# Performance work log

Hardware: AMD Instinct MI355X
Metric: run time of the kernel (lower is better)

## Reference

```python
import jax, jax.numpy as jnp
import numpy as np

T, B, I, H, O = 512, 64, 256, 512, 256

def setup_inputs() -> dict:
    key = jax.random.key(0)
    ks = jax.random.split(key, 7)
    s_ih = 1.0 / np.sqrt(H)
    return {
        "x": jax.random.normal(ks[0], (T, B, I), dtype=jnp.float32),
        "W_ih": jax.random.uniform(ks[1], (H, I), jnp.float32, -s_ih, s_ih),
        "W_hh": jax.random.uniform(ks[2], (H, H), jnp.float32, -s_ih, s_ih),
        "b_ih": jax.random.uniform(ks[3], (H,), jnp.float32, -s_ih, s_ih),
        "b_hh": jax.random.uniform(ks[4], (H,), jnp.float32, -s_ih, s_ih),
        "W_out": jax.random.uniform(ks[5], (O, H), jnp.float32, -s_ih, s_ih),
        "b_out": jax.random.uniform(ks[6], (O,), jnp.float32, -s_ih, s_ih),
    }

def reference(x, W_ih, W_hh, b_ih, b_hh, W_out, b_out):
    # Precompute input projection for all timesteps: [T, B, H]
    xp = jnp.einsum('tbi,hi->tbh', x, W_ih) + b_ih + b_hh

    def step(h, xp_t):
        h_new = jnp.tanh(xp_t + h @ W_hh.T)
        return h_new, h_new

    h0 = jnp.zeros((x.shape[1], W_hh.shape[0]), dtype=x.dtype)
    h_last, rnn_out = jax.lax.scan(step, h0, xp)  # rnn_out: [T, B, H]
    y = jnp.einsum('tbh,oh->tbo', rnn_out, W_out) + b_out
    return y, h_last[None]  # h: [1, B, H] matching torch nn.RNN
```

## Files before the change

kernel.cpp:

```cpp
#include <hip/hip_runtime.h>

#define T_DIM 512
#define B_DIM 64
#define I_DIM 256
#define H_DIM 512
#define O_DIM 256

typedef __attribute__((ext_vector_type(8))) short short8;
typedef __attribute__((ext_vector_type(4))) float f32x4;

__device__ __forceinline__ unsigned short f2bf(float f){
  unsigned int u = __builtin_bit_cast(unsigned int, f);
  u += 0x7fffu + ((u >> 16) & 1u);
  return (unsigned short)(u >> 16);
}
__device__ __forceinline__ float bf2f(unsigned short b){
  unsigned int u = ((unsigned int)b) << 16;
  return __builtin_bit_cast(float, u);
}

#if defined(__has_builtin)
#if __has_builtin(__builtin_amdgcn_sdot4)
#define HAVE_SDOT4 1
#endif
#if __has_builtin(__builtin_amdgcn_update_dpp)
#define HAVE_DPP 1
#endif
#endif

__device__ __forceinline__ int sdot4(int a, int b, int c){
#ifdef HAVE_SDOT4
  return __builtin_amdgcn_sdot4(a, b, c, false);
#else
  #pragma unroll
  for (int i = 0; i < 4; ++i){
    c += (int)(signed char)(a >> (8*i) & 0xff) * (int)(signed char)(b >> (8*i) & 0xff);
  }
  return c;
#endif
}

__device__ __forceinline__ int grp8_sum(int v){
#ifdef HAVE_DPP
  v += __builtin_amdgcn_update_dpp(0, v, 0xB1, 0xf, 0xf, true);
  v += __builtin_amdgcn_update_dpp(0, v, 0x4E, 0xf, 0xf, true);
  v += __builtin_amdgcn_update_dpp(0, v, 0x141, 0xf, 0xf, true);
  return v;
#else
  v += __shfl_xor(v, 1);
  v += __shfl_xor(v, 2);
  v += __shfl_xor(v, 4);
  return v;
#endif
}

__global__ void quant_whh(const float* __restrict__ W, int* __restrict__ Wq){
  int p = blockIdx.x * blockDim.x + threadIdx.x;
  const float s  = 0.04419417382415922f;
  const float qs = 127.0f / s;
  int out = 0;
  #pragma unroll
  for (int i = 0; i < 4; ++i){
    float w = W[(size_t)p*4 + i];
    int q = __float2int_rn(w * qs);
    q = q < -127 ? -127 : (q > 127 ? 127 : q);
    out |= (q & 0xff) << (8*i);
  }
  Wq[p] = out;
}

#define PIN16(i) asm volatile("" \
  : "+v"(w[i][ 0]), "+v"(w[i][ 1]), "+v"(w[i][ 2]), "+v"(w[i][ 3]), \
    "+v"(w[i][ 4]), "+v"(w[i][ 5]), "+v"(w[i][ 6]), "+v"(w[i][ 7]), \
    "+v"(w[i][ 8]), "+v"(w[i][ 9]), "+v"(w[i][10]), "+v"(w[i][11]), \
    "+v"(w[i][12]), "+v"(w[i][13]), "+v"(w[i][14]), "+v"(w[i][15]))

__global__
__attribute__((amdgpu_flat_work_group_size(512, 512), amdgpu_waves_per_eu(2, 2)))
void rnn_recur(
    const int* __restrict__ Wq,
    const unsigned short* __restrict__ xp,
    unsigned short* __restrict__ rnn,
    float* __restrict__ hlast)
{
  __shared__ union {
    int  hq[2][128];
    char occupancy_cap[84 * 1024];
  } sm;
  const int b   = blockIdx.x;
  const int tid = threadIdx.x;
  const int g   = tid >> 3;
  const int c   = tid & 7;

  int w[8][16];
  #pragma unroll
  for (int i = 0; i < 8; ++i){
    const uint4* wp = (const uint4*)(Wq + (size_t)(8*g + i)*128 + c*16);
    #pragma unroll
    for (int k = 0; k < 4; ++k){
      uint4 v = wp[k];
      w[i][4*k+0] = (int)v.x; w[i][4*k+1] = (int)v.y;
      w[i][4*k+2] = (int)v.z; w[i][4*k+3] = (int)v.w;
    }
  }
  if (tid < 256) ((int*)sm.hq)[tid] = 0;

  const int D = tid >> 2;
  const int wq_idx = ((D >> 4) + 8*((D >> 2) & 3))*4 + (D & 3);

  const float kscale = 0.04419417382415922f / (127.0f * 127.0f);
  const int BH = B_DIM * H_DIM;

  float xp_next = bf2f(xp[(size_t)b*H_DIM + tid]);
  __syncthreads();

  for (int t = 0; t < T_DIM; ++t){
    PIN16(0); PIN16(1); PIN16(2); PIN16(3);
    PIN16(4); PIN16(5); PIN16(6); PIN16(7);

    float xp_cur = xp_next;
    {
      int tn = (t + 1 < T_DIM) ? (t + 1) : t;
      xp_next = bf2f(xp[(size_t)tn*BH + (size_t)b*H_DIM + tid]);
    }
    const uint4* hb = (const uint4*)sm.hq[t & 1];
    uint4 hv0 = hb[c];
    uint4 hv1 = hb[c + 8];
    uint4 hv2 = hb[c + 16];
    uint4 hv3 = hb[c + 24];

    int acc[8];
    #pragma unroll
    for (int i = 0; i < 8; ++i) acc[i] = 0;
    #pragma unroll
    for (int i = 0; i < 8; ++i){
      acc[i] = sdot4(w[i][ 0], (int)hv0.x, acc[i]);
      acc[i] = sdot4(w[i][ 1], (int)hv0.y, acc[i]);
      acc[i] = sdot4(w[i][ 2], (int)hv0.z, acc[i]);
      acc[i] = sdot4(w[i][ 3], (int)hv0.w, acc[i]);
      acc[i] = sdot4(w[i][ 4], (int)hv1.x, acc[i]);
      acc[i] = sdot4(w[i][ 5], (int)hv1.y, acc[i]);
      acc[i] = sdot4(w[i][ 6], (int)hv1.z, acc[i]);
      acc[i] = sdot4(w[i][ 7], (int)hv1.w, acc[i]);
      acc[i] = sdot4(w[i][ 8], (int)hv2.x, acc[i]);
      acc[i] = sdot4(w[i][ 9], (int)hv2.y, acc[i]);
      acc[i] = sdot4(w[i][10], (int)hv2.z, acc[i]);
      acc[i] = sdot4(w[i][11], (int)hv2.w, acc[i]);
      acc[i] = sdot4(w[i][12], (int)hv3.x, acc[i]);
      acc[i] = sdot4(w[i][13], (int)hv3.y, acc[i]);
      acc[i] = sdot4(w[i][14], (int)hv3.z, acc[i]);
      acc[i] = sdot4(w[i][15], (int)hv3.w, acc[i]);
    }
    #pragma unroll
    for (int i = 0; i < 8; ++i) acc[i] = grp8_sum(acc[i]);

    int t0 = (c & 1) ? acc[1] : acc[0];
    int t1 = (c & 1) ? acc[3] : acc[2];
    int t2 = (c & 1) ? acc[5] : acc[4];
    int t3 = (c & 1) ? acc[7] : acc[6];
    int u0 = (c & 2) ? t1 : t0;
    int u1 = (c & 2) ? t3 : t2;
    int am = (c & 4) ? u1 : u0;

    float pre = xp_cur + (float)am * kscale;
    float aa = fabsf(pre);
    float e  = __expf(-2.0f * aa);
    float r  = (1.0f - e) * __builtin_amdgcn_rcpf(1.0f + e);
    float h  = copysignf(r, pre);

    rnn[(size_t)t*BH + (size_t)b*H_DIM + tid] = f2bf(h);
    if (t == T_DIM - 1) hlast[(size_t)b*H_DIM + tid] = h;

    int q = __float2int_rn(h * 127.0f) & 0xff;
#ifdef HAVE_DPP
    int p1 = __builtin_amdgcn_update_dpp(0, q, 0xB1, 0xf, 0xf, true);
    int y  = q | (p1 << 8);
    int p2 = __builtin_amdgcn_update_dpp(0, y, 0x4E, 0xf, 0xf, true);
    int z  = y | (p2 << 16);
    if ((tid & 3) == 0) sm.hq[(t + 1) & 1][wq_idx] = z;
#else
    ((char*)sm.hq[(t + 1) & 1])[wq_idx*4 + (tid & 3)] = (char)q;
#endif
    __syncthreads();
  }
}

template<typename TA, typename TB, typename TO>
__global__ __launch_bounds__(256) void gemm_bt(
    const TA* __restrict__ A, const TB* __restrict__ B, TO* __restrict__ C,
    const float* __restrict__ bias1, const float* __restrict__ bias2,
    int M, int N, int K)
{
  __shared__ unsigned short As[64][40];
  __shared__ unsigned short Bs[64][40];
  const int tid  = threadIdx.x;
  const int m0   = blockIdx.x * 64;
  const int n0   = blockIdx.y * 64;
  const int srow = tid >> 2, skc = tid & 3;
  const int lane = tid & 63, wid = tid >> 6;
  const int wm   = wid >> 1, wn = wid & 1;
  const int lr   = lane & 15, lq = lane >> 4;

  f32x4 acc[2][2];
  #pragma unroll
  for (int i = 0; i < 2; ++i)
    #pragma unroll
    for (int j = 0; j < 2; ++j) acc[i][j] = (f32x4){0.f, 0.f, 0.f, 0.f};

  for (int k0 = 0; k0 < K; k0 += 32){
    {
      const TA* src = A + (size_t)(m0 + srow)*K + k0 + skc*8;
      uint4 v;
      if constexpr (__is_same(TA, float)){
        float4 f0 = *(const float4*)src;
        float4 f1 = *(const float4*)(src + 4);
        v.x = (unsigned)f2bf(f0.x) | ((unsigned)f2bf(f0.y) << 16);
        v.y = (unsigned)f2bf(f0.z) | ((unsigned)f2bf(f0.w) << 16);
        v.z = (unsigned)f2bf(f1.x) | ((unsigned)f2bf(f1.y) << 16);
        v.w = (unsigned)f2bf(f1.z) | ((unsigned)f2bf(f1.w) << 16);
      } else {
        v = *(const uint4*)src;
      }
      *(uint4*)&As[srow][skc*8] = v;
    }
    {
      const TB* src = B + (size_t)(n0 + srow)*K + k0 + skc*8;
      uint4 v;
      if constexpr (__is_same(TB, float)){
        float4 f0 = *(const float4*)src;
        float4 f1 = *(const float4*)(src + 4);
        v.x = (unsigned)f2bf(f0.x) | ((unsigned)f2bf(f0.y) << 16);
        v.y = (unsigned)f2bf(f0.z) | ((unsigned)f2bf(f0.w) << 16);
        v.z = (unsigned)f2bf(f1.x) | ((unsigned)f2bf(f1.y) << 16);
        v.w = (unsigned)f2bf(f1.z) | ((unsigned)f2bf(f1.w) << 16);
      } else {
        v = *(const uint4*)src;
      }
      *(uint4*)&Bs[srow][skc*8] = v;
    }
    __syncthreads();
    uint4 av0 = *(const uint4*)&As[wm*32      + lr][lq*8];
    uint4 av1 = *(const uint4*)&As[wm*32 + 16 + lr][lq*8];
    uint4 bv0 = *(const uint4*)&Bs[wn*32      + lr][lq*8];
    uint4 bv1 = *(const uint4*)&Bs[wn*32 + 16 + lr][lq*8];
    short8 a0 = __builtin_bit_cast(short8, av0);
    short8 a1 = __builtin_bit_cast(short8, av1);
    short8 b0 = __builtin_bit_cast(short8, bv0);
    short8 b1 = __builtin_bit_cast(short8, bv1);
    acc[0][0] = __builtin_amdgcn_mfma_f32_16x16x32_bf16(a0, b0, acc[0][0], 0, 0, 0);
    acc[0][1] = __builtin_amdgcn_mfma_f32_16x16x32_bf16(a0, b1, acc[0][1], 0, 0, 0);
    acc[1][0] = __builtin_amdgcn_mfma_f32_16x16x32_bf16(a1, b0, acc[1][0], 0, 0, 0);
    acc[1][1] = __builtin_amdgcn_mfma_f32_16x16x32_bf16(a1, b1, acc[1][1], 0, 0, 0);
    __syncthreads();
  }

  #pragma unroll
  for (int i = 0; i < 2; ++i)
    #pragma unroll
    for (int j = 0; j < 2; ++j)
      #pragma unroll
      for (int r = 0; r < 4; ++r){
        int grow = m0 + wm*32 + i*16 + lq*4 + r;
        int gcol = n0 + wn*32 + j*16 + lr;
        float v = acc[i][j][r] + bias1[gcol];
        if (bias2) v += bias2[gcol];
        if constexpr (__is_same(TO, float)) C[(size_t)grow*N + gcol] = v;
        else                                C[(size_t)grow*N + gcol] = f2bf(v);
      }
}

extern "C" void kernel_launch(void* const* d_in, const int* in_sizes, int n_in,
                              void* d_out, int out_size, void* d_ws, size_t ws_size,
                              hipStream_t stream){
  (void)in_sizes; (void)n_in; (void)out_size; (void)ws_size;
  const float* x    = (const float*)d_in[0];
  const float* Wih  = (const float*)d_in[1];
  const float* Whh  = (const float*)d_in[2];
  const float* bih  = (const float*)d_in[3];
  const float* bhh  = (const float*)d_in[4];
  const float* Wout = (const float*)d_in[5];
  const float* bout = (const float*)d_in[6];
  float* y     = (float*)d_out;
  float* hlast = y + (size_t)T_DIM * B_DIM * O_DIM;

  char* ws = (char*)d_ws;
  unsigned short* xp  = (unsigned short*)ws;
  unsigned short* rnn = (unsigned short*)(ws + (size_t)32*1024*1024);
  int*            Wq  = (int*)           (ws + (size_t)64*1024*1024);

  quant_whh<<<256, 256, 0, stream>>>(Whh, Wq);
  gemm_bt<float, float, unsigned short><<<dim3(512, 8), 256, 0, stream>>>(
      x, Wih, xp, bih, bhh, T_DIM*B_DIM, H_DIM, I_DIM);
  rnn_recur<<<64, 512, 0, stream>>>(Wq, xp, rnn, hlast);
  gemm_bt<unsigned short, float, float><<<dim3(512, 4), 256, 0, stream>>>(
      rnn, Wout, y, bout, nullptr, T_DIM*B_DIM, O_DIM, H_DIM);
}
```

Measured before the change: 539.9 us.

## Split recurrence across 1024 threads with four W_hh rows per group

The recurrent kernel now launches 1024 threads per batch block instead of 512. Each 8-lane group holds four quantized W_hh rows instead of eight, which halves register pressure and the serial sdot4 chain each thread runs per timestep. The register pinning asm, the waves-per-eu attribute and the LDS padding that capped occupancy are removed. The cost is that half the lanes compute redundant outputs, and each block-wide barrier now spans twice as many waves on every step.

```diff
diff --git a/kernel.cpp b/kernel.cpp
--- a/kernel.cpp
+++ b/kernel.cpp
@@ -69,33 +69,25 @@
   Wq[p] = out;
 }
 
-#define PIN16(i) asm volatile("" \
-  : "+v"(w[i][ 0]), "+v"(w[i][ 1]), "+v"(w[i][ 2]), "+v"(w[i][ 3]), \
-    "+v"(w[i][ 4]), "+v"(w[i][ 5]), "+v"(w[i][ 6]), "+v"(w[i][ 7]), \
-    "+v"(w[i][ 8]), "+v"(w[i][ 9]), "+v"(w[i][10]), "+v"(w[i][11]), \
-    "+v"(w[i][12]), "+v"(w[i][13]), "+v"(w[i][14]), "+v"(w[i][15]))
-
 __global__
-__attribute__((amdgpu_flat_work_group_size(512, 512), amdgpu_waves_per_eu(2, 2)))
+__attribute__((amdgpu_flat_work_group_size(1024, 1024)))
 void rnn_recur(
     const int* __restrict__ Wq,
     const unsigned short* __restrict__ xp,
     unsigned short* __restrict__ rnn,
     float* __restrict__ hlast)
 {
-  __shared__ union {
-    int  hq[2][128];
-    char occupancy_cap[84 * 1024];
-  } sm;
+  __shared__ int hq[2][128];
   const int b   = blockIdx.x;
   const int tid = threadIdx.x;
   const int g   = tid >> 3;
   const int c   = tid & 7;
-
-  int w[8][16];
-  #pragma unroll
-  for (int i = 0; i < 8; ++i){
-    const uint4* wp = (const uint4*)(Wq + (size_t)(8*g + i)*128 + c*16);
+  const int row = 4*g + (c & 3);
+
+  int w[4][16];
+  #pragma unroll
+  for (int i = 0; i < 4; ++i){
+    const uint4* wp = (const uint4*)(Wq + (size_t)(4*g + i)*128 + c*16);
     #pragma unroll
     for (int k = 0; k < 4; ++k){
       uint4 v = wp[k];
@@ -103,37 +95,33 @@
       w[i][4*k+2] = (int)v.z; w[i][4*k+3] = (int)v.w;
     }
   }
-  if (tid < 256) ((int*)sm.hq)[tid] = 0;
-
-  const int D = tid >> 2;
-  const int wq_idx = ((D >> 4) + 8*((D >> 2) & 3))*4 + (D & 3);
+  if (tid < 128) hq[0][tid] = 0;
+
+  const int wj = 4*(g >> 4) + 32*((g >> 2) & 3) + (g & 3);
 
   const float kscale = 0.04419417382415922f / (127.0f * 127.0f);
   const int BH = B_DIM * H_DIM;
 
-  float xp_next = bf2f(xp[(size_t)b*H_DIM + tid]);
+  float xp_next = bf2f(xp[(size_t)b*H_DIM + row]);
   __syncthreads();
 
   for (int t = 0; t < T_DIM; ++t){
-    PIN16(0); PIN16(1); PIN16(2); PIN16(3);
-    PIN16(4); PIN16(5); PIN16(6); PIN16(7);
-
     float xp_cur = xp_next;
     {
       int tn = (t + 1 < T_DIM) ? (t + 1) : t;
-      xp_next = bf2f(xp[(size_t)tn*BH + (size_t)b*H_DIM + tid]);
-    }
-    const uint4* hb = (const uint4*)sm.hq[t & 1];
+      xp_next = bf2f(xp[(size_t)tn*BH + (size_t)b*H_DIM + row]);
+    }
+    const uint4* hb = (const uint4*)hq[t & 1];
     uint4 hv0 = hb[c];
     uint4 hv1 = hb[c + 8];
     uint4 hv2 = hb[c + 16];
     uint4 hv3 = hb[c + 24];
 
-    int acc[8];
-    #pragma unroll
-    for (int i = 0; i < 8; ++i) acc[i] = 0;
-    #pragma unroll
-    for (int i = 0; i < 8; ++i){
+    int acc[4];
+    #pragma unroll
+    for (int i = 0; i < 4; ++i) acc[i] = 0;
+    #pragma unroll
+    for (int i = 0; i < 4; ++i){
       acc[i] = sdot4(w[i][ 0], (int)hv0.x, acc[i]);
       acc[i] = sdot4(w[i][ 1], (int)hv0.y, acc[i]);
       acc[i] = sdot4(w[i][ 2], (int)hv0.z, acc[i]);
@@ -152,15 +140,11 @@
       acc[i] = sdot4(w[i][15], (int)hv3.w, acc[i]);
     }
     #pragma unroll
-    for (int i = 0; i < 8; ++i) acc[i] = grp8_sum(acc[i]);
+    for (int i = 0; i < 4; ++i) acc[i] = grp8_sum(acc[i]);
 
     int t0 = (c & 1) ? acc[1] : acc[0];
     int t1 = (c & 1) ? acc[3] : acc[2];
-    int t2 = (c & 1) ? acc[5] : acc[4];
-    int t3 = (c & 1) ? acc[7] : acc[6];
-    int u0 = (c & 2) ? t1 : t0;
-    int u1 = (c & 2) ? t3 : t2;
-    int am = (c & 4) ? u1 : u0;
+    int am = (c & 2) ? t1 : t0;
 
     float pre = xp_cur + (float)am * kscale;
     float aa = fabsf(pre);
@@ -168,8 +152,10 @@
     float r  = (1.0f - e) * __builtin_amdgcn_rcpf(1.0f + e);
     float h  = copysignf(r, pre);
 
-    rnn[(size_t)t*BH + (size_t)b*H_DIM + tid] = f2bf(h);
-    if (t == T_DIM - 1) hlast[(size_t)b*H_DIM + tid] = h;
+    if ((tid & 7) < 4){
+      rnn[(size_t)t*BH + (size_t)b*H_DIM + row] = f2bf(h);
+      if (t == T_DIM - 1) hlast[(size_t)b*H_DIM + row] = h;
+    }
 
     int q = __float2int_rn(h * 127.0f) & 0xff;
 #ifdef HAVE_DPP
@@ -177,9 +163,9 @@
     int y  = q | (p1 << 8);
     int p2 = __builtin_amdgcn_update_dpp(0, y, 0x4E, 0xf, 0xf, true);
     int z  = y | (p2 << 16);
-    if ((tid & 3) == 0) sm.hq[(t + 1) & 1][wq_idx] = z;
+    if ((tid & 7) == 0) hq[(t + 1) & 1][wj] = z;
 #else
-    ((char*)sm.hq[(t + 1) & 1])[wq_idx*4 + (tid & 3)] = (char)q;
+    if ((tid & 7) < 4) ((char*)hq[(t + 1) & 1])[wj*4 + c] = (char)q;
 #endif
     __syncthreads();
   }
@@ -291,7 +277,7 @@
   quant_whh<<<256, 256, 0, stream>>>(Whh, Wq);
   gemm_bt<float, float, unsigned short><<<dim3(512, 8), 256, 0, stream>>>(
       x, Wih, xp, bih, bhh, T_DIM*B_DIM, H_DIM, I_DIM);
-  rnn_recur<<<64, 512, 0, stream>>>(Wq, xp, rnn, hlast);
+  rnn_recur<<<64, 1024, 0, stream>>>(Wq, xp, rnn, hlast);
   gemm_bt<unsigned short, float, float><<<dim3(512, 4), 256, 0, stream>>>(
       rnn, Wout, y, bout, nullptr, T_DIM*B_DIM, O_DIM, H_DIM);
 }
```

New measurement: 601.1 us. +11.3%, slower.
